# Optimization experiments

Measured on AMD Instinct MI355X. Metric: run time of the kernel, lower is better.

## Reference

```python
import jax, jax.numpy as jnp
import numpy as np

TEMP = 1.0  # softmax temperature (init kwarg)


def setup_inputs() -> dict:
    key = jax.random.key(0)
    k1, k2 = jax.random.split(key)
    two_n, d_model = 512, 256
    embeddings = jax.random.normal(k1, (two_n, d_model), dtype=jnp.float32)
    targets = jax.random.uniform(k2, (two_n, 1), dtype=jnp.float32)
    return {"embeddings": embeddings, "targets": targets}


def reference(embeddings, targets):
    # embeddings: [2N, d_model], targets: [2N, 1]
    two_n = embeddings.shape[0]
    # label distance d[i,j] = |t_i - t_j|
    d = jnp.abs(targets - targets.T)                                  # [2N, 2N]
    # exp similarity s[i,j] = exp(-||e_i - e_j||_2 / temp)
    diff = embeddings[:, None, :] - embeddings[None, :, :]            # [2N, 2N, d]
    s = jnp.exp(-jnp.linalg.norm(diff, axis=-1) / TEMP)               # [2N, 2N]
    off_diag = 1.0 - jnp.eye(two_n, dtype=s.dtype)                    # [2N, 2N]
    # mask3[i,k,j] = (d[i,j] >= d[i,k]) * (j != i)
    mask3 = (d[:, None, :] >= d[:, :, None]).astype(s.dtype) * off_diag[:, None, :]
    # denominator D[i,k] = sum_j mask3[i,k,j] * s[i,j]
    denom = jnp.einsum('ikj,ij->ik', mask3, s)                        # [2N, 2N]
    loss = jnp.log(s / denom) * off_diag
    return -jnp.sum(loss) / (two_n * (two_n - 1))
```

## Files before the change

### kernel.cpp

```cpp
#include <hip/hip_runtime.h>
#include <math.h>

#define TWO_N 512
#define DM    256
#define NT    256

#define OFF_TSORT 1048576
#define OFF_PERM  1050624
#define OFF_INV   1052672
#define OFF_BSUM  1054720

#define ACC4(acc, A, B) { float _d;                      \
    _d = (A).x - (B).x; acc += _d * _d;                  \
    _d = (A).y - (B).y; acc += _d * _d;                  \
    _d = (A).z - (B).z; acc += _d * _d;                  \
    _d = (A).w - (B).w; acc += _d * _d; }

__global__ __launch_bounds__(NT) void supcr_dist_sort(
    const float* __restrict__ E, const float* __restrict__ T,
    float* __restrict__ R, float* __restrict__ tsort,
    int* __restrict__ perm, int* __restrict__ inv)
{
    const int bid = blockIdx.x;
    const int t   = threadIdx.x;

    if (bid < 256) {
        __shared__ float4 As4[32 * 65];
        __shared__ float4 Bs4[32 * 65];
        const int it = bid >> 4, jt = bid & 15;
        const float4* __restrict__ E4 = reinterpret_cast<const float4*>(E);

        for (int idx = t; idx < 32 * 64; idx += NT) {
            const int row = idx >> 6, c4 = idx & 63;
            As4[row * 65 + c4] = E4[(it * 32 + row) * 64 + c4];
            Bs4[row * 65 + c4] = E4[(jt * 32 + row) * 64 + c4];
        }
        __syncthreads();

        const int ty = t >> 4, tx = t & 15;
        float a00 = 0.f, a01 = 0.f, a10 = 0.f, a11 = 0.f;
        #pragma unroll 8
        for (int k4 = 0; k4 < 64; ++k4) {
            const float4 a0 = As4[ty * 65 + k4];
            const float4 a1 = As4[(ty + 16) * 65 + k4];
            const float4 b0 = Bs4[tx * 65 + k4];
            const float4 b1 = Bs4[(tx + 16) * 65 + k4];
            ACC4(a00, a0, b0); ACC4(a01, a0, b1);
            ACC4(a10, a1, b0); ACC4(a11, a1, b1);
        }
        const int r0 = it * 32 + ty, r1 = r0 + 16;
        const int c0 = jt * 32 + tx, c1 = c0 + 16;
        R[r0 * TWO_N + c0] = sqrtf(a00);
        R[r0 * TWO_N + c1] = sqrtf(a01);
        R[r1 * TWO_N + c0] = sqrtf(a10);
        R[r1 * TWO_N + c1] = sqrtf(a11);
    } else {
        __shared__ float key[TWO_N];
        __shared__ int   pay[TWO_N];
        key[t] = T[t]; key[t + 256] = T[t + 256];
        pay[t] = t;    pay[t + 256] = t + 256;
        __syncthreads();
        for (int kk = 2; kk <= TWO_N; kk <<= 1) {
            for (int j = kk >> 1; j > 0; j >>= 1) {
                #pragma unroll
                for (int w = 0; w < 2; ++w) {
                    const int e = t + w * 256;
                    const int p = e ^ j;
                    if (p > e) {
                        const float a = key[e], b = key[p];
                        const int  pa = pay[e], pb = pay[p];
                        const bool up = ((e & kk) == 0);
                        if (up ? (a > b) : (a < b)) {
                            key[e] = b; key[p] = a;
                            pay[e] = pb; pay[p] = pa;
                        }
                    }
                }
                __syncthreads();
            }
        }
        tsort[t] = key[t];           tsort[t + 256] = key[t + 256];
        perm[t]  = pay[t];           perm[t + 256]  = pay[t + 256];
        inv[pay[t]] = t;             inv[pay[t + 256]] = t + 256;
    }
}

__global__ __launch_bounds__(NT) void supcr_rows(
    const float* __restrict__ T, const float* __restrict__ R,
    const float* __restrict__ tsort, const int* __restrict__ perm,
    const int* __restrict__ inv, double* __restrict__ bsums)
{
    const int i = blockIdx.x;
    const int t = threadIdx.x;

    __shared__ float  ts[TWO_N];
    __shared__ float  P[TWO_N];
    __shared__ double red[NT];

    const float ti = T[i];

    #pragma unroll
    for (int w = 0; w < 2; ++w) {
        const int m = t + w * 256;
        ts[m] = tsort[m];
        const int pj = perm[m];
        P[m] = (pj == i) ? 0.f : __expf(-R[(size_t)i * TWO_N + pj]);
    }
    __syncthreads();

    for (int off = 1; off < TWO_N; off <<= 1) {
        const float v0 = (t >= off)       ? P[t - off]       : 0.f;
        const float v1 = (t + 256 >= off) ? P[t + 256 - off] : 0.f;
        __syncthreads();
        P[t]       += v0;
        P[t + 256] += v1;
        __syncthreads();
    }

    const float Stot = P[TWO_N - 1];
    const int   mi   = inv[i];

    float local = 0.f;
    #pragma unroll
    for (int w = 0; w < 2; ++w) {
        const int k = t + w * 256;
        if (k == i) continue;
        const float theta = fabsf(ti - T[k]);
        const float rik   = R[(size_t)i * TWO_N + k];

        const int nl = mi + 1;
        int pos = 0;
        #pragma unroll
        for (int step = 512; step >= 1; step >>= 1) {
            const int np = pos + step;
            if (np <= nl && fabsf(ti - ts[np - 1]) >= theta) pos = np;
        }
        const int cl = nl - pos;

        const int nr = TWO_N - mi;
        int pr = 0;
        #pragma unroll
        for (int step = 512; step >= 1; step >>= 1) {
            const int np = pr + step;
            if (np <= nr && fabsf(ti - ts[mi + np - 1]) < theta) pr = np;
        }
        const int cr = pr;

        float inner = 0.f;
        const int L  = mi - cl + 1;
        const int Rr = mi + cr - 1;
        if (Rr >= L) inner = P[Rr] - ((L > 0) ? P[L - 1] : 0.f);
        const float denom = Stot - inner;
        local += -rik - logf(denom);
    }

    red[t] = (double)local;
    __syncthreads();
    for (int off = NT / 2; off > 0; off >>= 1) {
        if (t < off) red[t] += red[t + off];
        __syncthreads();
    }
    if (t == 0) bsums[i] = red[0];
}

__global__ __launch_bounds__(TWO_N) void supcr_finalize(
    const double* __restrict__ bsums, float* __restrict__ out)
{
    __shared__ double red[TWO_N];
    const int t = threadIdx.x;
    red[t] = bsums[t];
    __syncthreads();
    for (int off = TWO_N / 2; off > 0; off >>= 1) {
        if (t < off) red[t] += red[t + off];
        __syncthreads();
    }
    if (t == 0)
        out[0] = (float)(-red[0] / (double)((long long)TWO_N * (TWO_N - 1)));
}

extern "C" void kernel_launch(void* const* d_in, const int* in_sizes, int n_in,
                              void* d_out, int out_size, void* d_ws, size_t ws_size,
                              hipStream_t stream) {
    (void)in_sizes; (void)n_in; (void)out_size; (void)ws_size;
    const float* E = (const float*)d_in[0];
    const float* T = (const float*)d_in[1];
    float* out = (float*)d_out;

    char* ws = (char*)d_ws;
    float*  R      = (float*)(ws);
    float*  tsortp = (float*)(ws + OFF_TSORT);
    int*    permp  = (int*)(ws + OFF_PERM);
    int*    invp   = (int*)(ws + OFF_INV);
    double* bsums  = (double*)(ws + OFF_BSUM);

    supcr_dist_sort<<<257, NT, 0, stream>>>(E, T, R, tsortp, permp, invp);
    supcr_rows<<<TWO_N, NT, 0, stream>>>(T, R, tsortp, permp, invp, bsums);
    supcr_finalize<<<1, TWO_N, 0, stream>>>(bsums, out);
}
```

Before: 78.15 us.

## Replace bitonic sort with rank counting, write distances permuted, fuse finalize via atomics

The single-block bitonic sort is replaced by a rank-counting sort. Every distance block recomputes the ranks of its columns, so distance rows are written directly in sorted order. The row kernel then reads rows contiguously instead of gathering through the permutation. The separate finalize kernel is removed: per-row sums go through double atomicAdd plus a completion counter, and the last block writes the result. This saves one launch and the long serial sort, but adds redundant O(N) rank work in every block and makes the summation order nondeterministic.

```diff
diff --git a/kernel.cpp b/kernel.cpp
--- a/kernel.cpp
+++ b/kernel.cpp
@@ -5,10 +5,10 @@
 #define DM    256
 #define NT    256
 
-#define OFF_TSORT 1048576
-#define OFF_PERM  1050624
-#define OFF_INV   1052672
-#define OFF_BSUM  1054720
+#define OFF_TS   1048576
+#define OFF_INV  1050624
+#define OFF_ACC  1052672
+#define OFF_CNT  1052680
 
 #define ACC4(acc, A, B) { float _d;                      \
     _d = (A).x - (B).x; acc += _d * _d;                  \
@@ -18,22 +18,53 @@
 
 __global__ __launch_bounds__(NT) void supcr_dist_sort(
     const float* __restrict__ E, const float* __restrict__ T,
-    float* __restrict__ R, float* __restrict__ tsort,
-    int* __restrict__ perm, int* __restrict__ inv)
+    float* __restrict__ Rp, float* __restrict__ ts_g, int* __restrict__ inv_g,
+    double* __restrict__ accum, unsigned int* __restrict__ count)
 {
     const int bid = blockIdx.x;
     const int t   = threadIdx.x;
 
+    __shared__ float tv[TWO_N];
+    tv[t]       = T[t];
+    tv[t + 256] = T[t + 256];
+    __syncthreads();
+
     if (bid < 256) {
         __shared__ float4 As4[32 * 65];
         __shared__ float4 Bs4[32 * 65];
+        __shared__ int    cnt[32 * 9];
+        __shared__ int    invc_s[32];
+
         const int it = bid >> 4, jt = bid & 15;
+
+        {
+            const int cl = t >> 3;
+            const int ss = t & 7;
+            const int c  = jt * 32 + cl;
+            const float tc = tv[c];
+            int n = 0;
+            const int j0 = ss * 64;
+            #pragma unroll 8
+            for (int j = j0; j < j0 + 64; ++j) {
+                const float tj = tv[j];
+                n += (tj < tc) || (tj == tc && j < c);
+            }
+            cnt[cl * 9 + ss] = n;
+        }
+
         const float4* __restrict__ E4 = reinterpret_cast<const float4*>(E);
-
         for (int idx = t; idx < 32 * 64; idx += NT) {
             const int row = idx >> 6, c4 = idx & 63;
             As4[row * 65 + c4] = E4[(it * 32 + row) * 64 + c4];
             Bs4[row * 65 + c4] = E4[(jt * 32 + row) * 64 + c4];
+        }
+        __syncthreads();
+
+        if (t < 32) {
+            int r = 0;
+            #pragma unroll
+            for (int ss = 0; ss < 8; ++ss) r += cnt[t * 9 + ss];
+            invc_s[t] = r;
         }
         __syncthreads();
 
@@ -49,62 +80,54 @@
             ACC4(a10, a1, b0); ACC4(a11, a1, b1);
         }
         const int r0 = it * 32 + ty, r1 = r0 + 16;
-        const int c0 = jt * 32 + tx, c1 = c0 + 16;
-        R[r0 * TWO_N + c0] = sqrtf(a00);
-        R[r0 * TWO_N + c1] = sqrtf(a01);
-        R[r1 * TWO_N + c0] = sqrtf(a10);
-        R[r1 * TWO_N + c1] = sqrtf(a11);
+        const int m0 = invc_s[tx],  m1 = invc_s[tx + 16];
+        Rp[r0 * TWO_N + m0] = sqrtf(a00);
+        Rp[r0 * TWO_N + m1] = sqrtf(a01);
+        Rp[r1 * TWO_N + m0] = sqrtf(a10);
+        Rp[r1 * TWO_N + m1] = sqrtf(a11);
     } else {
-        __shared__ float key[TWO_N];
-        __shared__ int   pay[TWO_N];
-        key[t] = T[t]; key[t + 256] = T[t + 256];
-        pay[t] = t;    pay[t + 256] = t + 256;
-        __syncthreads();
-        for (int kk = 2; kk <= TWO_N; kk <<= 1) {
-            for (int j = kk >> 1; j > 0; j >>= 1) {
-                #pragma unroll
-                for (int w = 0; w < 2; ++w) {
-                    const int e = t + w * 256;
-                    const int p = e ^ j;
-                    if (p > e) {
-                        const float a = key[e], b = key[p];
-                        const int  pa = pay[e], pb = pay[p];
-                        const bool up = ((e & kk) == 0);
-                        if (up ? (a > b) : (a < b)) {
-                            key[e] = b; key[p] = a;
-                            pay[e] = pb; pay[p] = pa;
-                        }
-                    }
-                }
-                __syncthreads();
+        #pragma unroll
+        for (int w = 0; w < 2; ++w) {
+            const int c  = t + w * 256;
+            const float tc = tv[c];
+            int r = 0;
+            #pragma unroll 8
+            for (int j = 0; j < TWO_N; ++j) {
+                const float tj = tv[j];
+                r += (tj < tc) || (tj == tc && j < c);
             }
-        }
-        tsort[t] = key[t];           tsort[t + 256] = key[t + 256];
-        perm[t]  = pay[t];           perm[t + 256]  = pay[t + 256];
-        inv[pay[t]] = t;             inv[pay[t + 256]] = t + 256;
+            ts_g[r]  = tc;
+            inv_g[c] = r;
+        }
+        if (t == 0) { *accum = 0.0; *count = 0u; }
     }
 }
 
 __global__ __launch_bounds__(NT) void supcr_rows(
-    const float* __restrict__ T, const float* __restrict__ R,
-    const float* __restrict__ tsort, const int* __restrict__ perm,
-    const int* __restrict__ inv, double* __restrict__ bsums)
+    const float* __restrict__ T, const float* __restrict__ Rp,
+    const float* __restrict__ ts_g, const int* __restrict__ inv_g,
+    double* __restrict__ accum, unsigned int* __restrict__ count,
+    float* __restrict__ out)
 {
     const int i = blockIdx.x;
     const int t = threadIdx.x;
 
     __shared__ float  ts[TWO_N];
+    __shared__ float  rv[TWO_N];
     __shared__ float  P[TWO_N];
     __shared__ double red[NT];
 
+    const int   mi = inv_g[i];
     const float ti = T[i];
+    const float* __restrict__ row = Rp + (size_t)i * TWO_N;
 
     #pragma unroll
     for (int w = 0; w < 2; ++w) {
         const int m = t + w * 256;
-        ts[m] = tsort[m];
-        const int pj = perm[m];
-        P[m] = (pj == i) ? 0.f : __expf(-R[(size_t)i * TWO_N + pj]);
+        ts[m] = ts_g[m];
+        const float r = row[m];
+        rv[m] = r;
+        P[m]  = (m == mi) ? 0.f : __expf(-r);
     }
     __syncthreads();
 
@@ -118,15 +141,13 @@
     }
 
     const float Stot = P[TWO_N - 1];
-    const int   mi   = inv[i];
 
     float local = 0.f;
     #pragma unroll
     for (int w = 0; w < 2; ++w) {
-        const int k = t + w * 256;
-        if (k == i) continue;
-        const float theta = fabsf(ti - T[k]);
-        const float rik   = R[(size_t)i * TWO_N + k];
+        const int m = t + w * 256;
+        if (m == mi) continue;
+        const float theta = fabsf(ti - ts[m]);
 
         const int nl = mi + 1;
         int pos = 0;
@@ -144,14 +165,13 @@
             const int np = pr + step;
             if (np <= nr && fabsf(ti - ts[mi + np - 1]) < theta) pr = np;
         }
-        const int cr = pr;
-
+
+        const int L  = mi - cl + 1;
+        const int Rr = mi + pr - 1;
         float inner = 0.f;
-        const int L  = mi - cl + 1;
-        const int Rr = mi + cr - 1;
         if (Rr >= L) inner = P[Rr] - ((L > 0) ? P[L - 1] : 0.f);
         const float denom = Stot - inner;
-        local += -rik - logf(denom);
+        local += -rv[m] - logf(denom);
     }
 
     red[t] = (double)local;
@@ -160,22 +180,15 @@
         if (t < off) red[t] += red[t + off];
         __syncthreads();
     }
-    if (t == 0) bsums[i] = red[0];
-}
-
-__global__ __launch_bounds__(TWO_N) void supcr_finalize(
-    const double* __restrict__ bsums, float* __restrict__ out)
-{
-    __shared__ double red[TWO_N];
-    const int t = threadIdx.x;
-    red[t] = bsums[t];
-    __syncthreads();
-    for (int off = TWO_N / 2; off > 0; off >>= 1) {
-        if (t < off) red[t] += red[t + off];
-        __syncthreads();
-    }
-    if (t == 0)
-        out[0] = (float)(-red[0] / (double)((long long)TWO_N * (TWO_N - 1)));
+    if (t == 0) {
+        const double part = red[0];
+        const double old  = atomicAdd(accum, part);
+        const unsigned int done = atomicAdd(count, 1u);
+        if (done == TWO_N - 1) {
+            out[0] = (float)(-(old + part) /
+                             (double)((long long)TWO_N * (TWO_N - 1)));
+        }
+    }
 }
 
 extern "C" void kernel_launch(void* const* d_in, const int* in_sizes, int n_in,
@@ -187,13 +200,12 @@
     float* out = (float*)d_out;
 
     char* ws = (char*)d_ws;
-    float*  R      = (float*)(ws);
-    float*  tsortp = (float*)(ws + OFF_TSORT);
-    int*    permp  = (int*)(ws + OFF_PERM);
-    int*    invp   = (int*)(ws + OFF_INV);
-    double* bsums  = (double*)(ws + OFF_BSUM);
-
-    supcr_dist_sort<<<257, NT, 0, stream>>>(E, T, R, tsortp, permp, invp);
-    supcr_rows<<<TWO_N, NT, 0, stream>>>(T, R, tsortp, permp, invp, bsums);
-    supcr_finalize<<<1, TWO_N, 0, stream>>>(bsums, out);
+    float*        Rp    = (float*)(ws);
+    float*        ts_g  = (float*)(ws + OFF_TS);
+    int*          inv_g = (int*)(ws + OFF_INV);
+    double*       acc   = (double*)(ws + OFF_ACC);
+    unsigned int* cnt   = (unsigned int*)(ws + OFF_CNT);
+
+    supcr_dist_sort<<<257, NT, 0, stream>>>(E, T, Rp, ts_g, inv_g, acc, cnt);
+    supcr_rows<<<TWO_N, NT, 0, stream>>>(T, Rp, ts_g, inv_g, acc, cnt, out);
 }
```

Result: slower. 95.90 us (+22.7%).

## Replace bitonic sort with rank sort and fuse finalize via last-block atomic

Applied to the files above, without the earlier changes.

The single sorting block now computes each target's rank by counting smaller elements across all 512 values, replacing the barrier-heavy bitonic network. The separate finalize kernel is removed: each row block publishes its partial sum and increments a global counter, and the last block to arrive does the final reduction. The sort block resets the counter in the first kernel. This removes one kernel launch and many __syncthreads steps, at the cost of O(N^2) compare work in one block and atomic/fence overhead.

```diff
diff --git a/kernel.cpp b/kernel.cpp
--- a/kernel.cpp
+++ b/kernel.cpp
@@ -5,10 +5,11 @@
 #define DM    256
 #define NT    256
 
-#define OFF_TSORT 1048576
-#define OFF_PERM  1050624
-#define OFF_INV   1052672
-#define OFF_BSUM  1054720
+#define OFF_TS   1048576
+#define OFF_PERM 1050624
+#define OFF_INV  1052672
+#define OFF_BSUM 1054720
+#define OFF_CNT  1058816
 
 #define ACC4(acc, A, B) { float _d;                      \
     _d = (A).x - (B).x; acc += _d * _d;                  \
@@ -18,8 +19,9 @@
 
 __global__ __launch_bounds__(NT) void supcr_dist_sort(
     const float* __restrict__ E, const float* __restrict__ T,
-    float* __restrict__ R, float* __restrict__ tsort,
-    int* __restrict__ perm, int* __restrict__ inv)
+    float* __restrict__ R, float* __restrict__ ts_g,
+    int* __restrict__ perm_g, int* __restrict__ inv_g,
+    unsigned int* __restrict__ count)
 {
     const int bid = blockIdx.x;
     const int t   = threadIdx.x;
@@ -55,40 +57,33 @@
         R[r1 * TWO_N + c0] = sqrtf(a10);
         R[r1 * TWO_N + c1] = sqrtf(a11);
     } else {
-        __shared__ float key[TWO_N];
-        __shared__ int   pay[TWO_N];
-        key[t] = T[t]; key[t + 256] = T[t + 256];
-        pay[t] = t;    pay[t + 256] = t + 256;
-        __syncthreads();
-        for (int kk = 2; kk <= TWO_N; kk <<= 1) {
-            for (int j = kk >> 1; j > 0; j >>= 1) {
-                #pragma unroll
-                for (int w = 0; w < 2; ++w) {
-                    const int e = t + w * 256;
-                    const int p = e ^ j;
-                    if (p > e) {
-                        const float a = key[e], b = key[p];
-                        const int  pa = pay[e], pb = pay[p];
-                        const bool up = ((e & kk) == 0);
-                        if (up ? (a > b) : (a < b)) {
-                            key[e] = b; key[p] = a;
-                            pay[e] = pb; pay[p] = pa;
-                        }
-                    }
-                }
-                __syncthreads();
+        __shared__ float tv[TWO_N];
+        tv[t]       = T[t];
+        tv[t + 256] = T[t + 256];
+        __syncthreads();
+        #pragma unroll
+        for (int w = 0; w < 2; ++w) {
+            const int c  = t + w * 256;
+            const float tc = tv[c];
+            int r = 0;
+            #pragma unroll 8
+            for (int j = 0; j < TWO_N; ++j) {
+                const float tj = tv[j];
+                r += (tj < tc) || (tj == tc && j < c);
             }
-        }
-        tsort[t] = key[t];           tsort[t + 256] = key[t + 256];
-        perm[t]  = pay[t];           perm[t + 256]  = pay[t + 256];
-        inv[pay[t]] = t;             inv[pay[t + 256]] = t + 256;
+            ts_g[r]   = tc;
+            perm_g[r] = c;
+            inv_g[c]  = r;
+        }
+        if (t == 0) *count = 0u;
     }
 }
 
 __global__ __launch_bounds__(NT) void supcr_rows(
     const float* __restrict__ T, const float* __restrict__ R,
-    const float* __restrict__ tsort, const int* __restrict__ perm,
-    const int* __restrict__ inv, double* __restrict__ bsums)
+    const float* __restrict__ ts_g, const int* __restrict__ perm_g,
+    const int* __restrict__ inv_g, double* __restrict__ bsums,
+    unsigned int* __restrict__ count, float* __restrict__ out)
 {
     const int i = blockIdx.x;
     const int t = threadIdx.x;
@@ -96,15 +91,18 @@
     __shared__ float  ts[TWO_N];
     __shared__ float  P[TWO_N];
     __shared__ double red[NT];
-
+    __shared__ bool   last;
+
+    const int   mi = inv_g[i];
     const float ti = T[i];
+    const float* __restrict__ row = R + (size_t)i * TWO_N;
 
     #pragma unroll
     for (int w = 0; w < 2; ++w) {
         const int m = t + w * 256;
-        ts[m] = tsort[m];
-        const int pj = perm[m];
-        P[m] = (pj == i) ? 0.f : __expf(-R[(size_t)i * TWO_N + pj]);
+        ts[m] = ts_g[m];
+        const int pj = perm_g[m];
+        P[m] = (pj == i) ? 0.f : __expf(-row[pj]);
     }
     __syncthreads();
 
@@ -118,7 +116,6 @@
     }
 
     const float Stot = P[TWO_N - 1];
-    const int   mi   = inv[i];
 
     float local = 0.f;
     #pragma unroll
@@ -126,7 +123,7 @@
         const int k = t + w * 256;
         if (k == i) continue;
         const float theta = fabsf(ti - T[k]);
-        const float rik   = R[(size_t)i * TWO_N + k];
+        const float rik   = row[k];
 
         const int nl = mi + 1;
         int pos = 0;
@@ -144,11 +141,10 @@
             const int np = pr + step;
             if (np <= nr && fabsf(ti - ts[mi + np - 1]) < theta) pr = np;
         }
-        const int cr = pr;
-
+
+        const int L  = mi - cl + 1;
+        const int Rr = mi + pr - 1;
         float inner = 0.f;
-        const int L  = mi - cl + 1;
-        const int Rr = mi + cr - 1;
         if (Rr >= L) inner = P[Rr] - ((L > 0) ? P[L - 1] : 0.f);
         const float denom = Stot - inner;
         local += -rik - logf(denom);
@@ -160,22 +156,32 @@
         if (t < off) red[t] += red[t + off];
         __syncthreads();
     }
-    if (t == 0) bsums[i] = red[0];
-}
-
-__global__ __launch_bounds__(TWO_N) void supcr_finalize(
-    const double* __restrict__ bsums, float* __restrict__ out)
-{
-    __shared__ double red[TWO_N];
-    const int t = threadIdx.x;
-    red[t] = bsums[t];
+
+    if (t == 0) {
+        __hip_atomic_store(&bsums[i], red[0], __ATOMIC_RELAXED,
+                           __HIP_MEMORY_SCOPE_AGENT);
+        __threadfence();
+        const unsigned int done = atomicAdd(count, 1u);
+        __threadfence();
+        last = (done == TWO_N - 1);
+    }
     __syncthreads();
-    for (int off = TWO_N / 2; off > 0; off >>= 1) {
-        if (t < off) red[t] += red[t + off];
-        __syncthreads();
-    }
-    if (t == 0)
-        out[0] = (float)(-red[0] / (double)((long long)TWO_N * (TWO_N - 1)));
+
+    if (last) {
+        double v0 = __hip_atomic_load(&bsums[t], __ATOMIC_ACQUIRE,
+                                      __HIP_MEMORY_SCOPE_AGENT);
+        double v1 = __hip_atomic_load(&bsums[t + 256], __ATOMIC_ACQUIRE,
+                                      __HIP_MEMORY_SCOPE_AGENT);
+        red[t] = v0 + v1;
+        __syncthreads();
+        for (int off = NT / 2; off > 0; off >>= 1) {
+            if (t < off) red[t] += red[t + off];
+            __syncthreads();
+        }
+        if (t == 0)
+            out[0] = (float)(-red[0] /
+                             (double)((long long)TWO_N * (TWO_N - 1)));
+    }
 }
 
 extern "C" void kernel_launch(void* const* d_in, const int* in_sizes, int n_in,
@@ -187,13 +193,13 @@
     float* out = (float*)d_out;
 
     char* ws = (char*)d_ws;
-    float*  R      = (float*)(ws);
-    float*  tsortp = (float*)(ws + OFF_TSORT);
-    int*    permp  = (int*)(ws + OFF_PERM);
-    int*    invp   = (int*)(ws + OFF_INV);
-    double* bsums  = (double*)(ws + OFF_BSUM);
-
-    supcr_dist_sort<<<257, NT, 0, stream>>>(E, T, R, tsortp, permp, invp);
-    supcr_rows<<<TWO_N, NT, 0, stream>>>(T, R, tsortp, permp, invp, bsums);
-    supcr_finalize<<<1, TWO_N, 0, stream>>>(bsums, out);
+    float*        R      = (float*)(ws);
+    float*        ts_g   = (float*)(ws + OFF_TS);
+    int*          perm_g = (int*)(ws + OFF_PERM);
+    int*          inv_g  = (int*)(ws + OFF_INV);
+    double*       bsums  = (double*)(ws + OFF_BSUM);
+    unsigned int* cnt    = (unsigned int*)(ws + OFF_CNT);
+
+    supcr_dist_sort<<<257, NT, 0, stream>>>(E, T, R, ts_g, perm_g, inv_g, cnt);
+    supcr_rows<<<TWO_N, NT, 0, stream>>>(T, R, ts_g, perm_g, inv_g, bsums, cnt, out);
 }
```

New measurement: 100.3 us. 28.3% more time.
